# Optimization experiments

Measured on AMD Instinct MI355X. Metric: run time of the kernel, lower is better.

## Reference

```python
import jax, jax.numpy as jnp
import numpy as np

TOP_K = 2

def setup_inputs() -> dict:
    key = jax.random.key(0)
    k1, k2 = jax.random.split(key)
    x = jax.random.normal(k1, (8, 4096, 4096), dtype=jnp.float32)
    # nn.Linear weight [num_experts, dim]
    gate_w = jax.random.normal(k2, (64, 4096), dtype=jnp.float32) * (1.0 / np.sqrt(4096))
    return {"x": x, "gate_w": gate_w}

def reference(x, gate_w):
    # logits: [B, S, E]
    logits = jnp.einsum('bsd,ed->bse', x, gate_w)
    routing_weights = jax.nn.softmax(logits, axis=-1)
    top_weights, top_indices = jax.lax.top_k(routing_weights, TOP_K)
    top_weights = top_weights / jnp.sum(top_weights, axis=-1, keepdims=True)
    return top_weights, top_indices
```

## Files before the change

kernel.cpp:

```cpp
#include <hip/hip_runtime.h>
#include <hip/hip_bf16.h>
#include <math.h>


typedef __attribute__((ext_vector_type(8))) short short8;
typedef __attribute__((ext_vector_type(4))) float f32x4;

#define TPB 128
#define NCH 64
#define TAU 1e-4f
#define LROW 68

__device__ __forceinline__ void cvt8(const f32x4* v, short8* hi, short8* lo) {
    const float* f = reinterpret_cast<const float*>(v);
#pragma unroll
    for (int j = 0; j < 8; ++j) {
        __hip_bfloat16 h = __float2bfloat16(f[j]);
        float r = f[j] - __bfloat162float(h);
        __hip_bfloat16 l = __float2bfloat16(r);
        (*hi)[j] = (short)*reinterpret_cast<unsigned short*>(&h);
        (*lo)[j] = (short)*reinterpret_cast<unsigned short*>(&l);
    }
}

__global__ void prep_b(const float* __restrict__ gw,
                       short8* __restrict__ bh, short8* __restrict__ bl) {
    const int tid = blockIdx.x * 256 + threadIdx.x;
    const int ln  = tid & 63;
    const int w   = (tid >> 6) & 127;
    const int nt  = tid >> 13;
    const int row = nt * 16 + (ln & 15);
    const int k   = w * 32 + ((ln >> 4) << 3);
    f32x4 v[2];
    v[0] = *reinterpret_cast<const f32x4*>(gw + (long)row * 4096 + k);
    v[1] = *reinterpret_cast<const f32x4*>(gw + (long)row * 4096 + k + 4);
    short8 h, l;
    cvt8(v, &h, &l);
    bh[tid] = h;
    bl[tid] = l;
}

__device__ __forceinline__ void gload16(const void* g, void* l) {
    __builtin_amdgcn_global_load_lds(
        (const __attribute__((address_space(1))) void*)g,
        (__attribute__((address_space(3))) void*)l, 16, 0, 0);
}

#define STAGE(C, BUF) do {                                                    \
    char* aB = AB + (BUF) * 49152;                                            \
    char* bB = aB + 32768;                                                    \
    _Pragma("unroll")                                                         \
    for (int i = 0; i < 4; ++i)                                               \
        gload16(srcA[i] + (long)(C) * 256, aB + (wv * 4 + i) * 1024 + ln * 16); \
    _Pragma("unroll")                                                         \
    for (int i = 0; i < 2; ++i) {                                             \
        const int s  = wv * 2 + i;                                            \
        const int wl = s >> 3, nt = (s >> 1) & 3, hl = s & 1;                 \
        const short8* sp = (hl ? blp : bhp)                                   \
            + ((long)nt * 8192 + (2 * (C) + wl) * 64 + ln);                   \
        gload16(sp, bB + s * 1024 + ln * 16);                                 \
    }                                                                         \
} while (0)

__global__ __launch_bounds__(512, 1)
void router_fused(const float* __restrict__ x,
                  const short8* __restrict__ bhp,
                  const short8* __restrict__ blp,
                  const float* __restrict__ gw,
                  float* __restrict__ out,
                  int M, int K) {
    __shared__ __align__(16) char AB[98304];
    __shared__ int flags[TPB];
    __shared__ double Ld4[4][64];

    const int t  = threadIdx.x;
    const int wv = t >> 6;
    const int ln = t & 63;
    const int fr = ln & 15;
    const int q  = ln >> 4;
    const long tok0 = (long)blockIdx.x * TPB;
    const int phase = blockIdx.x & (NCH - 1);

    const char* srcA[4];
#pragma unroll
    for (int i = 0; i < 4; ++i) {
        const int row  = (wv * 4 + i) * 4 + (ln >> 4);
        const int sl   = ln & 15;
        const int lslot = (sl & 8) | ((sl & 7) ^ (row & 7));
        srcA[i] = (const char*)x + (tok0 + row) * (long)K * 4 + lslot * 16;
    }

    f32x4 acc[4];
#pragma unroll
    for (int nt = 0; nt < 4; ++nt) acc[nt] = (f32x4){0.f, 0.f, 0.f, 0.f};

    STAGE(phase, 0);
    STAGE((phase + 1) & (NCH - 1), 1);

    const int R  = wv * 16 + fr;
    const int rk = R & 7;

    for (int j = 0; j < NCH; ++j) {
        const int c   = (phase + j) & (NCH - 1);
        const int buf = j & 1;
        if (j + 1 < NCH) asm volatile("s_waitcnt vmcnt(6)" ::: "memory");
        else             asm volatile("s_waitcnt vmcnt(0)" ::: "memory");
        __builtin_amdgcn_s_barrier();
        asm volatile("" ::: "memory");
        __builtin_amdgcn_sched_barrier(0);

        {
            const char* aB = AB + buf * 49152 + R * 256;
            const char* bB = AB + buf * 49152 + 32768;
#pragma unroll
            for (int wl = 0; wl < 2; ++wl) {
                f32x4 av[2];
                av[0] = *(const f32x4*)(aB + (wl * 8 + ((q * 2 + 0) ^ rk)) * 16);
                av[1] = *(const f32x4*)(aB + (wl * 8 + ((q * 2 + 1) ^ rk)) * 16);
                short8 ah, al;
                cvt8(av, &ah, &al);
#pragma unroll
                for (int nt = 0; nt < 4; ++nt) {
                    short8 bhv = *(const short8*)(bB + (wl * 8 + nt * 2 + 0) * 1024 + ln * 16);
                    short8 blv = *(const short8*)(bB + (wl * 8 + nt * 2 + 1) * 1024 + ln * 16);
                    acc[nt] = __builtin_amdgcn_mfma_f32_16x16x32_bf16(ah, bhv, acc[nt], 0, 0, 0);
                    acc[nt] = __builtin_amdgcn_mfma_f32_16x16x32_bf16(ah, blv, acc[nt], 0, 0, 0);
                    acc[nt] = __builtin_amdgcn_mfma_f32_16x16x32_bf16(al, bhv, acc[nt], 0, 0, 0);
                    acc[nt] = __builtin_amdgcn_mfma_f32_16x16x32_bf16(al, blv, acc[nt], 0, 0, 0);
                }
            }
        }

        __builtin_amdgcn_sched_barrier(0);
        asm volatile("" ::: "memory");
        __builtin_amdgcn_s_barrier();
        asm volatile("" ::: "memory");
        if (j + 2 < NCH) STAGE((phase + j + 2) & (NCH - 1), buf);
        __builtin_amdgcn_sched_barrier(0);
    }

    __syncthreads();
    float* Ls = (float*)AB;
#pragma unroll
    for (int nt = 0; nt < 4; ++nt)
#pragma unroll
        for (int r = 0; r < 4; ++r)
            Ls[(wv * 16 + q * 4 + r) * LROW + nt * 16 + fr] = acc[nt][r];
    __syncthreads();

    if (t < TPB) {
        const float* row = Ls + (long)t * LROW;
        float m1 = -INFINITY, m2 = -INFINITY, m3 = -INFINITY;
        int i1 = 0, i2 = 0;
#pragma unroll 8
        for (int e = 0; e < 64; ++e) {
            const float v = row[e];
            if (v > m1)      { m3 = m2; m2 = m1; i2 = i1; m1 = v; i1 = e; }
            else if (v > m2) { m3 = m2; m2 = v; i2 = e; }
            else if (v > m3) { m3 = v; }
        }
        const float e2 = expf(m2 - m1);
        const float s  = 1.0f + e2;

        const long g = tok0 + t;
        out[2 * g + 0] = 1.0f / s;
        out[2 * g + 1] = e2 / s;
        float* oi = out + 2 * (long)M;
        oi[2 * g + 0] = (float)i1;
        oi[2 * g + 1] = (float)i2;

        flags[t] = ((m1 - m2) < TAU) | ((m2 - m3) < TAU);
    }
    __syncthreads();

    for (int tk = 0; tk < TPB; ++tk) {
        if (flags[tk]) {
            if (t < 256) {
                const float* xr = x + (tok0 + tk) * (long)K + wv * 1024;
                const float* gr = gw + (long)ln * (long)K + wv * 1024;
                double s0 = 0.0, s1 = 0.0, s2 = 0.0, s3 = 0.0;
                for (int k = 0; k < 1024; k += 4) {
                    const f32x4 a = *reinterpret_cast<const f32x4*>(xr + k);
                    const f32x4 b = *reinterpret_cast<const f32x4*>(gr + k);
                    s0 = fma((double)a.x, (double)b.x, s0);
                    s1 = fma((double)a.y, (double)b.y, s1);
                    s2 = fma((double)a.z, (double)b.z, s2);
                    s3 = fma((double)a.w, (double)b.w, s3);
                }
                Ld4[wv][ln] = (s0 + s1) + (s2 + s3);
            }
            __syncthreads();
            if (t == 0) {
                double m1 = -INFINITY, m2 = -INFINITY;
                int i1 = 0, i2 = 0;
                for (int e = 0; e < 64; ++e) {
                    const double v = Ld4[0][e] + Ld4[1][e] + Ld4[2][e] + Ld4[3][e];
                    if (v > m1)      { m2 = m1; i2 = i1; m1 = v; i1 = e; }
                    else if (v > m2) { m2 = v; i2 = e; }
                }
                const double e2 = exp(m2 - m1);
                const double s  = 1.0 + e2;
                const long g = tok0 + tk;
                out[2 * g + 0] = (float)(1.0 / s);
                out[2 * g + 1] = (float)(e2 / s);
                float* oi = out + 2 * (long)M;
                oi[2 * g + 0] = (float)i1;
                oi[2 * g + 1] = (float)i2;
            }
            __syncthreads();
        }
    }
}

extern "C" void kernel_launch(void* const* d_in, const int* in_sizes, int n_in,
                              void* d_out, int out_size, void* d_ws, size_t ws_size,
                              hipStream_t stream) {
    const float* x  = (const float*)d_in[0];
    const float* gw = (const float*)d_in[1];
    float* out = (float*)d_out;

    const int K = 4096;
    const int M = in_sizes[0] / K;
    const int nblocks = M / TPB;

    short8* bh = (short8*)d_ws;
    short8* bl = bh + 32768;

    prep_b<<<128, 256, 0, stream>>>(gw, bh, bl);
    router_fused<<<nblocks, 512, 0, stream>>>(x, bh, bl, gw, out, M, K);
}
```

Baseline: 228.4 us.

## Switch router GEMM to fp16 split-A with single fp16 weights, smaller blocks

Replaces the bf16 hi/lo split on both operands (four MFMAs per tile) with an fp16 hi/lo split of the activations against a single fp16 copy of the gate weights (two MFMAs per tile). Halves the weight staging and LDS footprint, shrinks blocks to 256 threads and 64 tokens so up to three blocks can share a CU, and widens the near-tie threshold that triggers the fp64 recompute path. The aim is to cut MFMA and LDS work so the memory-bound x stream dominates. In exchange, the weights are rounded to fp16 (an approximation) and more tokens may fall back to the slow exact recompute.

```diff
diff --git a/kernel.cpp b/kernel.cpp
--- a/kernel.cpp
+++ b/kernel.cpp
@@ -1,43 +1,43 @@
 #include <hip/hip_runtime.h>
-#include <hip/hip_bf16.h>
+#include <hip/hip_fp16.h>
 #include <math.h>
 
 
 typedef __attribute__((ext_vector_type(8))) short short8;
 typedef __attribute__((ext_vector_type(4))) float f32x4;
 
-#define TPB 128
+#define TPB 64
 #define NCH 64
-#define TAU 1e-4f
+#define TAU 2e-3f
 #define LROW 68
 
-__device__ __forceinline__ void cvt8(const f32x4* v, short8* hi, short8* lo) {
+__device__ __forceinline__ void cvt8h(const f32x4* v, short8* hi, short8* lo) {
     const float* f = reinterpret_cast<const float*>(v);
 #pragma unroll
     for (int j = 0; j < 8; ++j) {
-        __hip_bfloat16 h = __float2bfloat16(f[j]);
-        float r = f[j] - __bfloat162float(h);
-        __hip_bfloat16 l = __float2bfloat16(r);
+        __half h = __float2half(f[j]);
+        float r = f[j] - __half2float(h);
+        __half l = __float2half(r);
         (*hi)[j] = (short)*reinterpret_cast<unsigned short*>(&h);
         (*lo)[j] = (short)*reinterpret_cast<unsigned short*>(&l);
     }
 }
 
-__global__ void prep_b(const float* __restrict__ gw,
-                       short8* __restrict__ bh, short8* __restrict__ bl) {
+__global__ void prep_h(const float* __restrict__ gw, short8* __restrict__ hp) {
     const int tid = blockIdx.x * 256 + threadIdx.x;
     const int ln  = tid & 63;
     const int w   = (tid >> 6) & 127;
     const int nt  = tid >> 13;
     const int row = nt * 16 + (ln & 15);
     const int k   = w * 32 + ((ln >> 4) << 3);
-    f32x4 v[2];
-    v[0] = *reinterpret_cast<const f32x4*>(gw + (long)row * 4096 + k);
-    v[1] = *reinterpret_cast<const f32x4*>(gw + (long)row * 4096 + k + 4);
-    short8 h, l;
-    cvt8(v, &h, &l);
-    bh[tid] = h;
-    bl[tid] = l;
+    const float* p = gw + (long)row * 4096 + k;
+    short8 h;
+#pragma unroll
+    for (int j = 0; j < 8; ++j) {
+        __half v = __float2half(p[j]);
+        h[j] = (short)*reinterpret_cast<unsigned short*>(&v);
+    }
+    hp[tid] = h;
 }
 
 __device__ __forceinline__ void gload16(const void* g, void* l) {
@@ -47,29 +47,27 @@
 }
 
 #define STAGE(C, BUF) do {                                                    \
-    char* aB = AB + (BUF) * 49152;                                            \
-    char* bB = aB + 32768;                                                    \
+    char* aB = AB + (BUF) * 24576;                                            \
+    char* bB = aB + 16384;                                                    \
     _Pragma("unroll")                                                         \
     for (int i = 0; i < 4; ++i)                                               \
         gload16(srcA[i] + (long)(C) * 256, aB + (wv * 4 + i) * 1024 + ln * 16); \
     _Pragma("unroll")                                                         \
     for (int i = 0; i < 2; ++i) {                                             \
         const int s  = wv * 2 + i;                                            \
-        const int wl = s >> 3, nt = (s >> 1) & 3, hl = s & 1;                 \
-        const short8* sp = (hl ? blp : bhp)                                   \
-            + ((long)nt * 8192 + (2 * (C) + wl) * 64 + ln);                   \
+        const int wl = s >> 2, nt = s & 3;                                    \
+        const short8* sp = hp + ((long)nt * 8192 + (2 * (C) + wl) * 64 + ln); \
         gload16(sp, bB + s * 1024 + ln * 16);                                 \
     }                                                                         \
 } while (0)
 
-__global__ __launch_bounds__(512, 1)
+__global__ __launch_bounds__(256, 3)
 void router_fused(const float* __restrict__ x,
-                  const short8* __restrict__ bhp,
-                  const short8* __restrict__ blp,
+                  const short8* __restrict__ hp,
                   const float* __restrict__ gw,
                   float* __restrict__ out,
                   int M, int K) {
-    __shared__ __align__(16) char AB[98304];
+    __shared__ __align__(16) char AB[49152];
     __shared__ int flags[TPB];
     __shared__ double Ld4[4][64];
 
@@ -103,6 +101,7 @@
     for (int j = 0; j < NCH; ++j) {
         const int c   = (phase + j) & (NCH - 1);
         const int buf = j & 1;
+        (void)c;
         if (j + 1 < NCH) asm volatile("s_waitcnt vmcnt(6)" ::: "memory");
         else             asm volatile("s_waitcnt vmcnt(0)" ::: "memory");
         __builtin_amdgcn_s_barrier();
@@ -110,23 +109,20 @@
         __builtin_amdgcn_sched_barrier(0);
 
         {
-            const char* aB = AB + buf * 49152 + R * 256;
-            const char* bB = AB + buf * 49152 + 32768;
+            const char* aB = AB + buf * 24576 + R * 256;
+            const char* bB = AB + buf * 24576 + 16384;
 #pragma unroll
             for (int wl = 0; wl < 2; ++wl) {
                 f32x4 av[2];
                 av[0] = *(const f32x4*)(aB + (wl * 8 + ((q * 2 + 0) ^ rk)) * 16);
                 av[1] = *(const f32x4*)(aB + (wl * 8 + ((q * 2 + 1) ^ rk)) * 16);
                 short8 ah, al;
-                cvt8(av, &ah, &al);
+                cvt8h(av, &ah, &al);
 #pragma unroll
                 for (int nt = 0; nt < 4; ++nt) {
-                    short8 bhv = *(const short8*)(bB + (wl * 8 + nt * 2 + 0) * 1024 + ln * 16);
-                    short8 blv = *(const short8*)(bB + (wl * 8 + nt * 2 + 1) * 1024 + ln * 16);
-                    acc[nt] = __builtin_amdgcn_mfma_f32_16x16x32_bf16(ah, bhv, acc[nt], 0, 0, 0);
-                    acc[nt] = __builtin_amdgcn_mfma_f32_16x16x32_bf16(ah, blv, acc[nt], 0, 0, 0);
-                    acc[nt] = __builtin_amdgcn_mfma_f32_16x16x32_bf16(al, bhv, acc[nt], 0, 0, 0);
-                    acc[nt] = __builtin_amdgcn_mfma_f32_16x16x32_bf16(al, blv, acc[nt], 0, 0, 0);
+                    short8 bv = *(const short8*)(bB + (wl * 4 + nt) * 1024 + ln * 16);
+                    acc[nt] = __builtin_amdgcn_mfma_f32_16x16x32_f16(ah, bv, acc[nt], 0, 0, 0);
+                    acc[nt] = __builtin_amdgcn_mfma_f32_16x16x32_f16(al, bv, acc[nt], 0, 0, 0);
                 }
             }
         }
@@ -175,20 +171,18 @@
 
     for (int tk = 0; tk < TPB; ++tk) {
         if (flags[tk]) {
-            if (t < 256) {
-                const float* xr = x + (tok0 + tk) * (long)K + wv * 1024;
-                const float* gr = gw + (long)ln * (long)K + wv * 1024;
-                double s0 = 0.0, s1 = 0.0, s2 = 0.0, s3 = 0.0;
-                for (int k = 0; k < 1024; k += 4) {
-                    const f32x4 a = *reinterpret_cast<const f32x4*>(xr + k);
-                    const f32x4 b = *reinterpret_cast<const f32x4*>(gr + k);
-                    s0 = fma((double)a.x, (double)b.x, s0);
-                    s1 = fma((double)a.y, (double)b.y, s1);
-                    s2 = fma((double)a.z, (double)b.z, s2);
-                    s3 = fma((double)a.w, (double)b.w, s3);
-                }
-                Ld4[wv][ln] = (s0 + s1) + (s2 + s3);
+            const float* xr = x + (tok0 + tk) * (long)K + wv * 1024;
+            const float* gr = gw + (long)ln * (long)K + wv * 1024;
+            double s0 = 0.0, s1 = 0.0, s2 = 0.0, s3 = 0.0;
+            for (int k = 0; k < 1024; k += 4) {
+                const f32x4 a = *reinterpret_cast<const f32x4*>(xr + k);
+                const f32x4 b = *reinterpret_cast<const f32x4*>(gr + k);
+                s0 = fma((double)a.x, (double)b.x, s0);
+                s1 = fma((double)a.y, (double)b.y, s1);
+                s2 = fma((double)a.z, (double)b.z, s2);
+                s3 = fma((double)a.w, (double)b.w, s3);
             }
+            Ld4[wv][ln] = (s0 + s1) + (s2 + s3);
             __syncthreads();
             if (t == 0) {
                 double m1 = -INFINITY, m2 = -INFINITY;
@@ -223,9 +217,8 @@
     const int M = in_sizes[0] / K;
     const int nblocks = M / TPB;
 
-    short8* bh = (short8*)d_ws;
-    short8* bl = bh + 32768;
-
-    prep_b<<<128, 256, 0, stream>>>(gw, bh, bl);
-    router_fused<<<nblocks, 512, 0, stream>>>(x, bh, bl, gw, out, M, K);
-}
+    short8* hp = (short8*)d_ws;
+
+    prep_h<<<128, 256, 0, stream>>>(gw, hp);
+    router_fused<<<nblocks, 256, 0, stream>>>(x, hp, gw, out, M, K);
+}
```

Result: slower. 429.3 us (+87.9%).
